# Performance work log

Hardware: AMD Instinct MI355X
Metric: run time of the kernel (lower is better)

## Reference

```python
import jax, jax.numpy as jnp
import numpy as np

B, S, H = 16, 2048, 768
HH = H // 2
C = 64          # num_concepts
L = 4           # num_labels
MIN_SPAN, MAX_SPAN = 3, 20
LEN_BONUS = 0.01
LN_EPS = 1e-5


def _ln(x, g, b):
    m = jnp.mean(x, axis=-1, keepdims=True)
    v = jnp.mean((x - m) ** 2, axis=-1, keepdims=True)
    return (x - m) * jax.lax.rsqrt(v + LN_EPS) * g + b


def _span_mask(scores, valid_len):
    """Vectorized replacement of the per-batch Python span-search loop.
    Replicates torch semantics: iterate span_len (small first), strict '>' update,
    torch.max returns first argmax -> equals argmax over flattened [K,S] array
    with span_len-major ordering."""
    b, s = scores.shape
    cum0 = jnp.concatenate([jnp.zeros((b, 1), scores.dtype),
                            jnp.cumsum(scores, axis=1)], axis=1)          # [B,S+1]
    Ls = jnp.arange(MIN_SPAN, MAX_SPAN + 1)                               # [K]
    starts = jnp.arange(s)                                                # [S]
    ends = starts[None, :] + Ls[:, None]                                  # [K,S]
    ends_c = jnp.minimum(ends, s)
    span_sum = cum0[:, ends_c] - cum0[:, starts][:, None, :]              # [B,K,S]
    avg = span_sum / Ls[None, :, None].astype(scores.dtype) \
        + LEN_BONUS * Ls[None, :, None].astype(scores.dtype) / MAX_SPAN
    valid = ends[None, :, :] <= valid_len[:, None, None]                  # start+len<=valid_len
    avg = jnp.where(valid, avg, -1e30)
    flat_idx = jnp.argmax(avg.reshape(b, -1), axis=1)                     # [B]
    l_idx, start = flat_idx // s, flat_idx % s
    length = Ls[l_idx]
    pos = jnp.arange(s)[None, :]
    span_m = (pos >= start[:, None]) & (pos < (start + length)[:, None])
    short_m = pos < valid_len[:, None]                                    # valid_len<=min_span case
    mask = jnp.where((valid_len <= MIN_SPAN)[:, None], short_m, span_m)
    return jax.lax.stop_gradient(mask.astype(scores.dtype))


def setup_inputs() -> dict:
    key = jax.random.key(0)
    ks = jax.random.split(key, 16)
    std = 0.02
    inp = {
        'inputs_embeds': jax.random.normal(ks[0], (B, S, H), jnp.float32),
        'attention_mask': jnp.ones((B, S), jnp.int32),
        # rationale extractor
        'Wq': jax.random.normal(ks[1], (H, HH), jnp.float32) * std,
        'bq': jnp.zeros((HH,), jnp.float32),
        'Wk': jax.random.normal(ks[2], (H, HH), jnp.float32) * std,
        'bk': jnp.zeros((HH,), jnp.float32),
        'W1': jax.random.normal(ks[3], (H, HH), jnp.float32) * std,
        'b1': jnp.zeros((HH,), jnp.float32),
        'g1': jnp.ones((HH,), jnp.float32),
        'be1': jnp.zeros((HH,), jnp.float32),
        'W2': jax.random.normal(ks[4], (HH, 1), jnp.float32) * 0.01,
        'b2': jnp.zeros((1,), jnp.float32),
        # concept mapper
        'Wc1': jax.random.normal(ks[5], (H, HH), jnp.float32) * std,
        'bc1': jnp.zeros((HH,), jnp.float32),
        'g2': jnp.ones((HH,), jnp.float32),
        'be2': jnp.zeros((HH,), jnp.float32),
        'Wc2': jax.random.normal(ks[6], (HH, C), jnp.float32) * std,
        'bc2': jnp.zeros((C,), jnp.float32),
        'Mint': jnp.zeros((C, C), jnp.float32),  # concept_interactions init zeros
        # classifier (skip connection -> C + H inputs)
        'Wcls': jax.random.normal(ks[7], (C + H, L), jnp.float32) * std,
        'bcls': jnp.zeros((L,), jnp.float32),
    }
    return inp


def reference(inputs_embeds, attention_mask, Wq, bq, Wk, bk, W1, b1, g1, be1, W2, b2,
              Wc1, bc1, g2, be2, Wc2, bc2, Mint, Wcls, bcls):
    x = inputs_embeds                                  # [B,S,H]
    am = attention_mask.astype(bool)                   # [B,S]
    cls_emb = x[:, 0]                                  # [B,H]

    # token scores via self-attention (eval mode: dropout = identity)
    q = x @ Wq + bq                                    # [B,S,HH]
    k = x @ Wk + bk
    attn = jnp.einsum('bsd,btd->bst', q, k) / jnp.sqrt(jnp.float32(HH))
    attn = jnp.where(am[:, None, :], attn, -10000.0)
    p = jax.nn.softmax(attn, axis=-1)
    ctx = jnp.einsum('bst,bth->bsh', p, x)             # [B,S,H]
    h = jax.nn.relu(_ln(ctx @ W1 + b1, g1, be1))
    token_scores = (h @ W2 + b2)[..., 0]               # [B,S]
    token_scores = jnp.where(am, token_scores, -10000.0)

    # span selection + masked mean pooling
    valid_len = jnp.sum(attention_mask.astype(jnp.int32), axis=1)
    rmask = _span_mask(token_scores, valid_len)        # [B,S]
    attended = x * rmask[..., None]
    pooled = jnp.sum(attended, axis=1) / (jnp.sum(rmask, axis=1, keepdims=True) + 1e-6)

    # concept mapper with interactions
    cs = jax.nn.relu(_ln(pooled @ Wc1 + bc1, g2, be2)) @ Wc2 + bc2   # [B,C]
    sym = jax.nn.sigmoid((Mint + Mint.T) / 2)
    cs = cs + cs @ sym
    cprobs = jax.nn.sigmoid(cs)

    logits = jnp.concatenate([cprobs, cls_emb], axis=1) @ Wcls + bcls  # [B,L]
    return logits
```

## Files before the change

kernel.cpp:

```cpp
#include <hip/hip_runtime.h>
#include <hip/hip_bf16.h>

#define Bn  16
#define Sn  2048
#define Hn  768
#define HHn 384

typedef unsigned short ushortT;
typedef unsigned int u32;
typedef __attribute__((ext_vector_type(8))) short short8;
typedef __attribute__((ext_vector_type(4))) short short4v;
typedef __attribute__((ext_vector_type(4))) float f32x4;

static constexpr float SCALE = 0.051031036307982884f;
static constexpr float EPS_PATCH = 0.025f;

static __device__ __forceinline__ float bf2f(ushortT u) {
    return __uint_as_float(((unsigned int)u) << 16);
}
static __device__ __forceinline__ ushortT f2bf(float f) {
    __hip_bfloat16 h = __float2bfloat16(f);
    return *reinterpret_cast<ushortT*>(&h);
}

static __device__ __forceinline__ void gld16(const void* g, void* l) {
    __builtin_amdgcn_global_load_lds(
        (const __attribute__((address_space(1))) u32*)g,
        (__attribute__((address_space(3))) u32*)l, 16, 0, 0);
}
static __device__ __forceinline__ void stage24k(const ushortT* g, unsigned char* l, int tid) {
    const int wid = tid >> 6, lane = tid & 63;
    const unsigned char* gp = (const unsigned char*)g;
#pragma unroll
    for (int i = 0; i < 6; ++i) {
        int blk = i * 4 + wid;
        gld16(gp + blk * 1024 + lane * 16, l + blk * 1024);
    }
}

__global__ __launch_bounds__(256) void convert_x(
    const float* __restrict__ X, ushortT* __restrict__ Xhi, ushortT* __restrict__ Xlo)
{
    size_t i = ((size_t)blockIdx.x * 256 + threadIdx.x) * 4;
    float4 v = *reinterpret_cast<const float4*>(&X[i]);
    short4v h, l;
    float vv[4] = {v.x, v.y, v.z, v.w};
#pragma unroll
    for (int j = 0; j < 4; ++j) {
        ushortT hb = f2bf(vv[j]);
        h[j] = (short)hb;
        l[j] = (short)f2bf(vv[j] - bf2f(hb));
    }
    *reinterpret_cast<short4v*>(&Xhi[i]) = h;
    *reinterpret_cast<short4v*>(&Xlo[i]) = l;
}

__global__ __launch_bounds__(256) void convert_w(
    const float* __restrict__ Wq, const float* __restrict__ Wk, const float* __restrict__ W1,
    ushortT* __restrict__ Wth, ushortT* __restrict__ Wtl)
{
    int t = blockIdx.x * 256 + threadIdx.x;
    int w = t / 36864;
    int r = t % 36864;
    int kg = r / 384;
    int n  = r % 384;
    const float* W = (w == 0) ? Wq : (w == 1) ? Wk : W1;
    short8 h, l;
#pragma unroll
    for (int j = 0; j < 8; ++j) {
        float v = W[(size_t)(kg * 8 + j) * HHn + n];
        ushortT hb = f2bf(v);
        h[j] = (short)hb;
        l[j] = (short)f2bf(v - bf2f(hb));
    }
    size_t off = (size_t)w * 294912 + (size_t)n * 768 + kg * 8;
    *reinterpret_cast<short8*>(&Wth[off]) = h;
    *reinterpret_cast<short8*>(&Wtl[off]) = l;
}

__global__ __launch_bounds__(256, 3) void proj_mfma(
    const ushortT* __restrict__ Xhi, const ushortT* __restrict__ Xlo,
    const ushortT* __restrict__ Wth, const ushortT* __restrict__ Wtl,
    const float* __restrict__ bq, const float* __restrict__ bk, const float* __restrict__ b1,
    ushortT* __restrict__ Qhi, ushortT* __restrict__ Khi, ushortT* __restrict__ Klo,
    ushortT* __restrict__ Uhi, ushortT* __restrict__ Ulo)
{
    __shared__ __align__(16) unsigned char smem[34816];

    const int wsel = blockIdx.z;
    const bool full = (wsel != 0);
    const float* bias = (wsel == 0) ? bq : (wsel == 1) ? bk : b1;
    const ushortT* Wh = Wth + (size_t)wsel * 294912;
    const ushortT* Wl = Wtl + (size_t)wsel * 294912;
    const int m0 = blockIdx.x * 128;
    const int n0 = blockIdx.y * 128;

    const int tid = threadIdx.x, wid = tid >> 6, lane = tid & 63;
    const int quad = lane >> 4, l15 = lane & 15;
    const int mw = (wid >> 1) * 64, nw = (wid & 1) * 64;
    const int r4 = lane >> 2, s2 = lane & 3;
    const int fs = (l15 >> 1) & 3;

    f32x4 acc[4][4];
#pragma unroll
    for (int mt = 0; mt < 4; ++mt)
#pragma unroll
        for (int nt = 0; nt < 4; ++nt) acc[mt][nt] = (f32x4){0.f, 0.f, 0.f, 0.f};

    for (int ks = 0; ks < 24; ++ks) {
        const int k0 = ks * 32;
        __syncthreads();
        {
            const int rb = wid * 32;
#pragma unroll
            for (int h = 0; h < 2; ++h) {
                int row = rb + h * 16 + r4;
                int sw = (row >> 1) & 3;
                size_t gsegA = (size_t)(m0 + row) * 768 + k0 + ((s2 ^ sw) << 3);
                size_t gsegB = (size_t)(n0 + row) * 768 + k0 + ((s2 ^ sw) << 3);
                gld16(&Xhi[gsegA], smem + (rb + h * 16) * 64);
                gld16(&Wh[gsegB],  smem + 16384 + (rb + h * 16) * 64);
                if (full) {
                    gld16(&Xlo[gsegA], smem + 8192  + (rb + h * 16) * 64);
                    gld16(&Wl[gsegB],  smem + 24576 + (rb + h * 16) * 64);
                }
            }
        }
        __syncthreads();

        short8 ah[4], bh[4], al[4], bl[4];
#pragma unroll
        for (int t = 0; t < 4; ++t) {
            int aaddr = (mw + t * 16 + l15) * 64 + ((quad ^ fs) << 4);
            int baddr = (nw + t * 16 + l15) * 64 + ((quad ^ fs) << 4);
            ah[t] = *reinterpret_cast<const short8*>(smem + aaddr);
            bh[t] = *reinterpret_cast<const short8*>(smem + 16384 + baddr);
            if (full) {
                al[t] = *reinterpret_cast<const short8*>(smem + 8192  + aaddr);
                bl[t] = *reinterpret_cast<const short8*>(smem + 24576 + baddr);
            }
        }
#pragma unroll
        for (int mt = 0; mt < 4; ++mt)
#pragma unroll
            for (int nt = 0; nt < 4; ++nt) {
                acc[mt][nt] = __builtin_amdgcn_mfma_f32_16x16x32_bf16(ah[mt], bh[nt], acc[mt][nt], 0, 0, 0);
                if (full) {
                    acc[mt][nt] = __builtin_amdgcn_mfma_f32_16x16x32_bf16(ah[mt], bl[nt], acc[mt][nt], 0, 0, 0);
                    acc[mt][nt] = __builtin_amdgcn_mfma_f32_16x16x32_bf16(al[mt], bh[nt], acc[mt][nt], 0, 0, 0);
                }
            }
    }
    __syncthreads();

    float bv[4];
#pragma unroll
    for (int nt = 0; nt < 4; ++nt) bv[nt] = bias[n0 + nw + nt * 16 + l15];

    if (wsel == 0) {
#pragma unroll
        for (int mt = 0; mt < 4; ++mt)
#pragma unroll
            for (int nt = 0; nt < 4; ++nt)
#pragma unroll
                for (int rg = 0; rg < 4; ++rg) {
                    float v = acc[mt][nt][rg] + bv[nt];
                    *reinterpret_cast<ushortT*>(smem + (mw + mt * 16 + quad * 4 + rg) * 272
                                                     + (nw + nt * 16 + l15) * 2) = f2bf(v);
                }
        __syncthreads();
#pragma unroll
        for (int i = 0; i < 8; ++i) {
            int idx = i * 256 + tid, ml = idx >> 4, cl = idx & 15;
            *reinterpret_cast<uint4*>(&Qhi[(size_t)(m0 + ml) * HHn + n0 + cl * 8]) =
                *reinterpret_cast<const uint4*>(smem + ml * 272 + cl * 16);
        }
    } else if (wsel == 1) {
#pragma unroll
        for (int pass = 0; pass < 2; ++pass) {
            if (pass) __syncthreads();
#pragma unroll
            for (int mt = 0; mt < 4; ++mt)
#pragma unroll
                for (int nt = 0; nt < 4; ++nt)
#pragma unroll
                    for (int rg = 0; rg < 4; ++rg) {
                        float v = acc[mt][nt][rg] + bv[nt];
                        ushortT hb = f2bf(v);
                        ushortT outw = pass ? f2bf(v - bf2f(hb)) : hb;
                        *reinterpret_cast<ushortT*>(smem + (mw + mt * 16 + quad * 4 + rg) * 272
                                                         + (nw + nt * 16 + l15) * 2) = outw;
                    }
            __syncthreads();
            ushortT* dst = pass ? Klo : Khi;
#pragma unroll
            for (int i = 0; i < 8; ++i) {
                int idx = i * 256 + tid, ml = idx >> 4, cl = idx & 15;
                int m = m0 + ml, bb2 = m >> 11, kg = m & 2047, kt = kg >> 6, key = kg & 63;
                int sc_ = ((n0 >> 3) + cl) ^ (key & 7);
                size_t off = ((size_t)(bb2 * 32 + kt) * 64 + key) * 384 + sc_ * 8;
                *reinterpret_cast<uint4*>(&dst[off]) =
                    *reinterpret_cast<const uint4*>(smem + ml * 272 + cl * 16);
            }
        }
    } else {
#pragma unroll
        for (int pass = 0; pass < 2; ++pass) {
            if (pass) __syncthreads();
#pragma unroll
            for (int mt = 0; mt < 4; ++mt)
#pragma unroll
                for (int nt = 0; nt < 4; ++nt) {
                    short4v pk;
#pragma unroll
                    for (int rg = 0; rg < 4; ++rg) {
                        float v = acc[mt][nt][rg] + bv[nt];
                        ushortT hb = f2bf(v);
                        pk[rg] = (short)(pass ? f2bf(v - bf2f(hb)) : hb);
                    }
                    *reinterpret_cast<short4v*>(smem + (nw + nt * 16 + l15) * 272
                                                     + (mw + mt * 16 + quad * 4) * 2) = pk;
                }
            __syncthreads();
            ushortT* dst = pass ? Ulo : Uhi;
#pragma unroll
            for (int i = 0; i < 8; ++i) {
                int idx = i * 256 + tid, dl = idx >> 4, ms = idx & 15;
                int dim = n0 + dl;
                int m = m0 + ms * 8, bb2 = m >> 11, tib = m & 2047;
                int kc = tib >> 5, k8 = (tib >> 3) & 3;
                int sk = k8 ^ (dim & 3);
                size_t off = ((size_t)(bb2 * 64 + kc) * 384 + dim) * 32 + sk * 8;
                *reinterpret_cast<uint4*>(&dst[off]) =
                    *reinterpret_cast<const uint4*>(smem + dl * 272 + ms * 16);
            }
        }
    }
}

__global__ __launch_bounds__(256) void proj_gemm(
    const float* __restrict__ X,
    const float* __restrict__ Wq, const float* __restrict__ bq,
    const float* __restrict__ Wk, const float* __restrict__ bk,
    const float* __restrict__ W1, const float* __restrict__ b1,
    ushortT* __restrict__ Qhi, ushortT* __restrict__ Khi, ushortT* __restrict__ Klo,
    ushortT* __restrict__ Uhi, ushortT* __restrict__ Ulo)
{
    const float* W; const float* bias;
    const int wsel = blockIdx.z;
    if (wsel == 0)      { W = Wq; bias = bq; }
    else if (wsel == 1) { W = Wk; bias = bk; }
    else                { W = W1; bias = b1; }

    const int m0  = blockIdx.x * 128;
    const int n0  = blockIdx.y * 128;
    const int tid = threadIdx.x;
    const int im  = tid >> 4;
    const int jn  = tid & 15;

    __shared__ __align__(16) float sA[16][132];
    __shared__ __align__(16) float sB[16][132];

    float acc[8][8];
#pragma unroll
    for (int i = 0; i < 8; ++i)
#pragma unroll
        for (int j = 0; j < 8; ++j) acc[i][j] = 0.f;

    for (int k0 = 0; k0 < Hn; k0 += 16) {
        __syncthreads();
#pragma unroll
        for (int it = 0; it < 2; ++it) {
            int f = tid + 256 * it;
            int row = f >> 2, k4 = (f & 3) * 4;
            float4 v = *reinterpret_cast<const float4*>(
                &X[(size_t)(m0 + row) * Hn + k0 + k4]);
            sA[k4 + 0][row] = v.x; sA[k4 + 1][row] = v.y;
            sA[k4 + 2][row] = v.z; sA[k4 + 3][row] = v.w;
        }
#pragma unroll
        for (int it = 0; it < 2; ++it) {
            int f = tid + 256 * it;
            int kk = f >> 5, n4 = (f & 31) * 4;
            *reinterpret_cast<float4*>(&sB[kk][n4]) =
                *reinterpret_cast<const float4*>(&W[(size_t)(k0 + kk) * HHn + n0 + n4]);
        }
        __syncthreads();
#pragma unroll
        for (int kk = 0; kk < 16; ++kk) {
            float a[8], bb[8];
            *reinterpret_cast<float4*>(&a[0])  = *reinterpret_cast<const float4*>(&sA[kk][im * 8]);
            *reinterpret_cast<float4*>(&a[4])  = *reinterpret_cast<const float4*>(&sA[kk][im * 8 + 4]);
            *reinterpret_cast<float4*>(&bb[0]) = *reinterpret_cast<const float4*>(&sB[kk][jn * 8]);
            *reinterpret_cast<float4*>(&bb[4]) = *reinterpret_cast<const float4*>(&sB[kk][jn * 8 + 4]);
#pragma unroll
            for (int i = 0; i < 8; ++i)
#pragma unroll
                for (int j = 0; j < 8; ++j) acc[i][j] += a[i] * bb[j];
        }
    }

    if (wsel == 0) {
#pragma unroll
        for (int i = 0; i < 8; ++i) {
            size_t m = (size_t)m0 + im * 8 + i;
            int nb = n0 + jn * 8;
            short8 hv;
#pragma unroll
            for (int j = 0; j < 8; ++j) hv[j] = (short)f2bf(acc[i][j] + bias[nb + j]);
            *reinterpret_cast<short8*>(&Qhi[m * HHn + nb]) = hv;
        }
    } else if (wsel == 1) {
        const int bb = m0 >> 11;
        const int bibase = m0 & 2047;
#pragma unroll
        for (int i = 0; i < 8; ++i) {
            int kg = bibase + im * 8 + i;
            int kt = kg >> 6, key = kg & 63;
            size_t rowoff = ((size_t)(bb * 32 + kt) * 64 + key) * 384;
            int sc_ = ((n0 >> 3) + jn) ^ (key & 7);
            short8 hv, lv;
#pragma unroll
            for (int j = 0; j < 8; ++j) {
                float v = acc[i][j] + bias[n0 + jn * 8 + j];
                ushortT hb = f2bf(v);
                hv[j] = (short)hb;
                lv[j] = (short)f2bf(v - bf2f(hb));
            }
            *reinterpret_cast<short8*>(&Khi[rowoff + sc_ * 8]) = hv;
            *reinterpret_cast<short8*>(&Klo[rowoff + sc_ * 8]) = lv;
        }
    } else {
        const int bb = m0 >> 11;
        const int tib = (m0 & 2047) + im * 8;
        const int kc = tib >> 5, k8 = (tib >> 3) & 3;
        const size_t cbase = (size_t)(bb * 64 + kc) * 384;
#pragma unroll
        for (int j = 0; j < 8; ++j) {
            int dim = n0 + jn * 8 + j;
            int sk = k8 ^ (dim & 3);
            float bvv = bias[dim];
            short8 hv, lv;
#pragma unroll
            for (int i = 0; i < 8; ++i) {
                float v = acc[i][j] + bvv;
                ushortT hb = f2bf(v);
                hv[i] = (short)hb;
                lv[i] = (short)f2bf(v - bf2f(hb));
            }
            size_t off = (cbase + dim) * 32 + sk * 8;
            *reinterpret_cast<short8*>(&Uhi[off]) = hv;
            *reinterpret_cast<short8*>(&Ulo[off]) = lv;
        }
    }
}

__global__ __launch_bounds__(256, 2) void attn_mfma(
    const ushortT* Qg, const ushortT* __restrict__ Kp, const ushortT* __restrict__ Up,
    const int* __restrict__ am, ushortT* Hp)
{
    __shared__ __align__(16) unsigned char smem[81920];
    ushortT* sP = (ushortT*)(smem + 73728);

    const int tid  = threadIdx.x;
    const int wid  = tid >> 6;
    const int lane = tid & 63;
    const int quad = lane >> 4;
    const int l15  = lane & 15;
    const int b    = blockIdx.y;
    const int q0   = blockIdx.x * 64;
    const size_t rowbase = (size_t)b * Sn + q0;
    const int* amb = am + b * Sn;

    const ushortT* Kbase = Kp + (size_t)b * 32 * 64 * 384;
    const ushortT* Ubase = Up + (size_t)b * 64 * 12288;

    const int r0 = wid * 16;
    short8 qf[12];
#pragma unroll
    for (int ks = 0; ks < 12; ++ks)
        qf[ks] = *reinterpret_cast<const short8*>(
            &Qg[(rowbase + r0 + l15) * HHn + ks * 32 + quad * 8]);

    f32x4 o[4][6];
#pragma unroll
    for (int rt = 0; rt < 4; ++rt)
#pragma unroll
        for (int dt = 0; dt < 6; ++dt) o[rt][dt] = (f32x4){0.f, 0.f, 0.f, 0.f};
    float denacc[4] = {0.f, 0.f, 0.f, 0.f};

    int ia = 0, ibx = 24576, ic = 49152;
    stage24k(Kbase, smem + ia, tid);
    stage24k(Kbase + 12288, smem + ibx, tid);
    __syncthreads();

    const int d0 = wid * 96;

    for (int kt = 0; kt < 32; ++kt) {
        stage24k(Ubase + (size_t)(kt * 2) * 12288, smem + ic, tid);

        f32x4 sc[4];
#pragma unroll
        for (int ct = 0; ct < 4; ++ct) sc[ct] = (f32x4){0.f, 0.f, 0.f, 0.f};
#pragma unroll
        for (int ks = 0; ks < 12; ++ks) {
#pragma unroll
            for (int ct = 0; ct < 4; ++ct) {
                int kl = (ct & 1) * 16 + l15;
                const unsigned char* Bk = smem + ((ct < 2) ? ia : ibx);
                short8 bf = *reinterpret_cast<const short8*>(
                    Bk + kl * 768 + ((((ks << 2) + quad) ^ (kl & 7)) << 4));
                sc[ct] = __builtin_amdgcn_mfma_f32_16x16x32_bf16(qf[ks], bf, sc[ct], 0, 0, 0);
            }
        }

        float dp[4] = {0.f, 0.f, 0.f, 0.f};
#pragma unroll
        for (int ct = 0; ct < 4; ++ct) {
            int col = ct * 16 + l15;
            float mval = (amb[kt * 64 + col] != 0) ? 1.f : 0.f;
#pragma unroll
            for (int rg = 0; rg < 4; ++rg) {
                int row = r0 + quad * 4 + rg;
                float p = __expf(sc[ct][rg] * SCALE) * mval;
                sP[row * 64 + (((col >> 3) ^ (row & 7)) << 3) + (col & 7)] = f2bf(p);
                dp[rg] += p;
            }
        }
#pragma unroll
        for (int off = 1; off < 16; off <<= 1)
#pragma unroll
            for (int rg = 0; rg < 4; ++rg) dp[rg] += __shfl_xor(dp[rg], off, 16);
#pragma unroll
        for (int rg = 0; rg < 4; ++rg) denacc[rg] += dp[rg];

        __syncthreads();

        stage24k(Ubase + (size_t)(kt * 2 + 1) * 12288, smem + ia, tid);
        if (kt < 31) stage24k(Kbase + (size_t)(kt + 1) * 24576, smem + ibx, tid);

        {
            const unsigned char* Bu = smem + ic;
            short8 pa[4];
#pragma unroll
            for (int rt = 0; rt < 4; ++rt)
                pa[rt] = *reinterpret_cast<const short8*>(
                    &sP[(16 * rt + l15) * 64 + ((quad ^ (l15 & 7)) << 3)]);
#pragma unroll
            for (int dt = 0; dt < 6; ++dt) {
                short8 u = *reinterpret_cast<const short8*>(
                    Bu + (d0 + 16 * dt + l15) * 64 + ((quad ^ (l15 & 3)) << 4));
#pragma unroll
                for (int rt = 0; rt < 4; ++rt)
                    o[rt][dt] = __builtin_amdgcn_mfma_f32_16x16x32_bf16(pa[rt], u, o[rt][dt], 0, 0, 0);
            }
        }
        __syncthreads();

        if (kt < 31) stage24k(Kbase + (size_t)(kt + 1) * 24576 + 12288, smem + ic, tid);

        {
            const unsigned char* Bu = smem + ia;
            short8 pa[4];
#pragma unroll
            for (int rt = 0; rt < 4; ++rt)
                pa[rt] = *reinterpret_cast<const short8*>(
                    &sP[(16 * rt + l15) * 64 + (((4 + quad) ^ (l15 & 7)) << 3)]);
#pragma unroll
            for (int dt = 0; dt < 6; ++dt) {
                short8 u = *reinterpret_cast<const short8*>(
                    Bu + (d0 + 16 * dt + l15) * 64 + ((quad ^ (l15 & 3)) << 4));
#pragma unroll
                for (int rt = 0; rt < 4; ++rt)
                    o[rt][dt] = __builtin_amdgcn_mfma_f32_16x16x32_bf16(pa[rt], u, o[rt][dt], 0, 0, 0);
            }
        }
        __syncthreads();

        int t = ia; ia = ibx; ibx = ic; ic = t;
    }

    float* sDenF = (float*)smem;
    if (l15 == 0) {
#pragma unroll
        for (int rg = 0; rg < 4; ++rg) sDenF[r0 + quad * 4 + rg] = denacc[rg];
    }
    __syncthreads();
    ushortT* sHp = (ushortT*)(smem + 512);
#pragma unroll
    for (int rt = 0; rt < 4; ++rt)
#pragma unroll
        for (int rg = 0; rg < 4; ++rg) {
            int row = rt * 16 + quad * 4 + rg;
            float inv = 1.f / sDenF[row];
#pragma unroll
            for (int dt = 0; dt < 6; ++dt)
                sHp[row * 384 + d0 + dt * 16 + l15] = f2bf(o[rt][dt][rg] * inv);
        }
    __syncthreads();
#pragma unroll
    for (int i = 0; i < 12; ++i) {
        int idx = i * 256 + tid;
        *reinterpret_cast<uint4*>(&Hp[rowbase * HHn + idx * 8]) =
            *reinterpret_cast<const uint4*>(&sHp[idx * 8]);
    }
}

__global__ __launch_bounds__(256) void ln_score_kernel(
    const ushortT* __restrict__ Hp, const float* __restrict__ g1, const float* __restrict__ be1,
    const float* __restrict__ W2, const float* __restrict__ b2,
    const int* __restrict__ am, float* __restrict__ scores, int* __restrict__ count)
{
    if (blockIdx.x == 0 && threadIdx.x == 0) *count = 0;
    const int row  = blockIdx.x * 4 + (threadIdx.x >> 6);
    const int lane = threadIdx.x & 63;
    const ushortT* x = Hp + (size_t)row * HHn;
    float v[6];
#pragma unroll
    for (int j = 0; j < 6; ++j) v[j] = bf2f(x[lane + 64 * j]);
    float s = 0.f;
#pragma unroll
    for (int j = 0; j < 6; ++j) s += v[j];
#pragma unroll
    for (int off = 32; off > 0; off >>= 1) s += __shfl_xor(s, off, 64);
    const float mean = s * (1.0f / 384.0f);
    float q = 0.f;
#pragma unroll
    for (int j = 0; j < 6; ++j) { float d = v[j] - mean; q += d * d; }
#pragma unroll
    for (int off = 32; off > 0; off >>= 1) q += __shfl_xor(q, off, 64);
    const float rstd = rsqrtf(q * (1.0f / 384.0f) + 1e-5f);
    float part = 0.f;
#pragma unroll
    for (int j = 0; j < 6; ++j) {
        int d = lane + 64 * j;
        float h = (v[j] - mean) * rstd * g1[d] + be1[d];
        h = fmaxf(h, 0.f);
        part += h * W2[d];
    }
#pragma unroll
    for (int off = 32; off > 0; off >>= 1) part += __shfl_xor(part, off, 64);
    if (lane == 0) {
        float scv = part + b2[0];
        if (am[row] == 0) scv = -10000.0f;
        scores[row] = scv;
    }
}

__global__ __launch_bounds__(256) void span_flag_kernel(
    const float* __restrict__ scores, const int* __restrict__ am,
    int* __restrict__ list, int* __restrict__ count)
{
    __shared__ float cum[Sn + 1];
    __shared__ float psum[257];
    __shared__ float bval[256];
    __shared__ int   sred[256];
    __shared__ int   sInfo[1];
    __shared__ float sBest;
    __shared__ unsigned char sflag[Sn];

    const int b = blockIdx.x, tid = threadIdx.x;
    for (int i = tid; i < Sn; i += 256) sflag[i] = 0;

    int vl = 0;
    for (int i = tid; i < Sn; i += 256) vl += am[b * Sn + i];
    sred[tid] = vl;
    __syncthreads();
    if (tid == 0) { int t = 0; for (int i = 0; i < 256; ++i) t += sred[i]; sInfo[0] = t; }
    __syncthreads();
    const int valid_len = sInfo[0];

    float loc[8]; float tot = 0.f;
#pragma unroll
    for (int k2 = 0; k2 < 8; ++k2) { loc[k2] = scores[b * Sn + tid * 8 + k2]; tot += loc[k2]; }
    psum[tid + 1] = tot;
    __syncthreads();
    if (tid == 0) {
        psum[0] = 0.f;
        float r = 0.f;
        for (int i = 1; i <= 256; ++i) { float t = psum[i]; psum[i] = r + t; r += t; }
    }
    __syncthreads();
    {
        float r = (tid == 0) ? 0.f : psum[tid];
        if (tid == 0) cum[0] = 0.f;
#pragma unroll
        for (int k2 = 0; k2 < 8; ++k2) { r += loc[k2]; cum[tid * 8 + k2 + 1] = r; }
    }
    __syncthreads();

    float bv = -3.0e30f;
    for (int flat = tid; flat < 18 * Sn; flat += 256) {
        int l = flat >> 11, st = flat & (Sn - 1), L = 3 + l, end = st + L;
        float val;
        if (end <= valid_len) {
            int ec = end < Sn ? end : Sn;
            val = (cum[ec] - cum[st]) / (float)L + (0.01f * (float)L) / 20.0f;
        } else val = -1.0e30f;
        if (val > bv) bv = val;
    }
    bval[tid] = bv;
    __syncthreads();
    if (tid == 0) {
        float best = bval[0];
        for (int i = 1; i < 256; ++i) if (bval[i] > best) best = bval[i];
        sBest = best;
    }
    __syncthreads();

    if (valid_len > 3) {
        const float thr = sBest - EPS_PATCH;
        for (int flat = tid; flat < 18 * Sn; flat += 256) {
            int l = flat >> 11, st = flat & (Sn - 1), L = 3 + l, end = st + L;
            if (end <= valid_len) {
                int ec = end < Sn ? end : Sn;
                float val = (cum[ec] - cum[st]) / (float)L + (0.01f * (float)L) / 20.0f;
                if (val >= thr)
                    for (int t = st; t < end; ++t) sflag[t] = 1;
            }
        }
        __syncthreads();
        for (int t = tid; t < Sn; t += 256)
            if (sflag[t]) { int idx = atomicAdd(count, 1); list[idx] = (b << 16) | t; }
    }
}

static __device__ __forceinline__ float block_sum256(float v, float* sws, int tid)
{
#pragma unroll
    for (int off = 32; off > 0; off >>= 1) v += __shfl_xor(v, off, 64);
    __syncthreads();
    if ((tid & 63) == 0) sws[tid >> 6] = v;
    __syncthreads();
    return sws[0] + sws[1] + sws[2] + sws[3];
}

__global__ __launch_bounds__(256) void patch_kernel(
    const int* __restrict__ list, const int* __restrict__ count,
    const float* __restrict__ X, const float* __restrict__ Wq, const float* __restrict__ bq,
    const ushortT* __restrict__ Khi, const ushortT* __restrict__ Klo,
    const ushortT* __restrict__ Uhi, const ushortT* __restrict__ Ulo,
    const float* __restrict__ g1, const float* __restrict__ be1,
    const float* __restrict__ W2, const float* __restrict__ b2,
    const int* __restrict__ am, float* __restrict__ scores)
{
    __shared__ float sx[Hn];
    __shared__ float sq[HHn];
    __shared__ float sp[Sn];
    __shared__ float sws[4];
    const int tid = threadIdx.x;
    const int n = *count;

    for (int li = blockIdx.x; li < n; li += gridDim.x) {
        int e = list[li];
        int b = e >> 16, t = e & 0xffff;
        __syncthreads();
        for (int d = tid; d < Hn; d += 256) sx[d] = X[((size_t)b * Sn + t) * Hn + d];
        __syncthreads();
        for (int d = tid; d < HHn; d += 256) {
            float a = bq[d];
            for (int k = 0; k < Hn; ++k) a += sx[k] * Wq[(size_t)k * HHn + d];
            sq[d] = a;
        }
        __syncthreads();
        float dpart = 0.f;
        for (int j = tid; j < Sn; j += 256) {
            float p = 0.f;
            if (am[b * Sn + j] != 0) {
                int kt = j >> 6, key = j & 63, kk7 = key & 7;
                size_t ro = ((size_t)(b * 32 + kt) * 64 + key) * 384;
                const ushortT* kh = &Khi[ro];
                const ushortT* kl = &Klo[ro];
                float s = 0.f;
                for (int c = 0; c < 48; ++c) {
                    int dbase = (c ^ kk7) << 3;
                    for (int ee = 0; ee < 8; ++ee)
                        s += sq[dbase + ee] * (bf2f(kh[c * 8 + ee]) + bf2f(kl[c * 8 + ee]));
                }
                p = expf(s * SCALE);
            }
            sp[j] = p; dpart += p;
        }
        const float den = block_sum256(dpart, sws, tid);

        float cown[2] = {0.f, 0.f};
        {
            int ii = 0;
            for (int d = tid; d < HHn; d += 256, ++ii) {
                int d3 = d & 3;
                float c = 0.f;
                for (int kc = 0; kc < 64; ++kc) {
                    size_t ub = ((size_t)(b * 64 + kc) * 384 + d) * 32;
                    const ushortT* uh = &Uhi[ub];
                    const ushortT* ul = &Ulo[ub];
                    for (int k8 = 0; k8 < 4; ++k8) {
                        int sk = k8 ^ d3;
                        int j0 = kc * 32 + k8 * 8;
                        for (int ee = 0; ee < 8; ++ee)
                            c += sp[j0 + ee] * (bf2f(uh[sk * 8 + ee]) + bf2f(ul[sk * 8 + ee]));
                    }
                }
                cown[ii] = c / den;
            }
        }
        float ssum = cown[0] + cown[1];
        const float mean = block_sum256(ssum, sws, tid) * (1.0f / 384.0f);
        float vsum = 0.f;
        {
            int ii = 0;
            for (int d = tid; d < HHn; d += 256, ++ii) {
                float dv = cown[ii] - mean; vsum += dv * dv;
            }
        }
        const float var = block_sum256(vsum, sws, tid) * (1.0f / 384.0f);
        const float rstd = rsqrtf(var + 1e-5f);
        float spart = 0.f;
        {
            int ii = 0;
            for (int d = tid; d < HHn; d += 256, ++ii) {
                float h = (cown[ii] - mean) * rstd * g1[d] + be1[d];
                h = fmaxf(h, 0.f);
                spart += h * W2[d];
            }
        }
        const float sc = block_sum256(spart, sws, tid) + b2[0];
        if (tid == 0)
            scores[b * Sn + t] = (am[b * Sn + t] != 0) ? sc : -10000.0f;
        __syncthreads();
    }
}

__global__ __launch_bounds__(256) void span_pool_kernel(
    const float* __restrict__ scores, const int* __restrict__ am,
    const float* __restrict__ X, float* __restrict__ pooled)
{
    __shared__ float cum[Sn + 1];
    __shared__ float psum[257];
    __shared__ float bval[256];
    __shared__ int   bidx[256];
    __shared__ int   sred[256];
    __shared__ int   sInfo[2];

    const int b = blockIdx.x, tid = threadIdx.x;

    int vl = 0;
    for (int i = tid; i < Sn; i += 256) vl += am[b * Sn + i];
    sred[tid] = vl;
    __syncthreads();
    if (tid == 0) { int t = 0; for (int i = 0; i < 256; ++i) t += sred[i]; sInfo[0] = t; }
    __syncthreads();
    const int valid_len = sInfo[0];

    float loc[8]; float tot = 0.f;
#pragma unroll
    for (int k2 = 0; k2 < 8; ++k2) { loc[k2] = scores[b * Sn + tid * 8 + k2]; tot += loc[k2]; }
    psum[tid + 1] = tot;
    __syncthreads();
    if (tid == 0) {
        psum[0] = 0.f;
        float r = 0.f;
        for (int i = 1; i <= 256; ++i) { float t = psum[i]; psum[i] = r + t; r += t; }
    }
    __syncthreads();
    {
        float r = (tid == 0) ? 0.f : psum[tid];
        if (tid == 0) cum[0] = 0.f;
#pragma unroll
        for (int k2 = 0; k2 < 8; ++k2) { r += loc[k2]; cum[tid * 8 + k2 + 1] = r; }
    }
    __syncthreads();

    float bv = -3.0e30f; int bi = 0x7fffffff;
    for (int flat = tid; flat < 18 * Sn; flat += 256) {
        int l  = flat >> 11;
        int st = flat & (Sn - 1);
        int L  = 3 + l;
        int end = st + L;
        float val;
        if (end <= valid_len) {
            int ec = end < Sn ? end : Sn;
            val = (cum[ec] - cum[st]) / (float)L + (0.01f * (float)L) / 20.0f;
        } else val = -1.0e30f;
        if (val > bv) { bv = val; bi = flat; }
    }
    bval[tid] = bv; bidx[tid] = bi;
    __syncthreads();
    if (tid == 0) {
        float best = bval[0]; int besti = bidx[0];
        for (int i = 1; i < 256; ++i) {
            if (bval[i] > best || (bval[i] == best && bidx[i] < besti)) {
                best = bval[i]; besti = bidx[i];
            }
        }
        int st, len;
        if (valid_len <= 3) { st = 0; len = valid_len; }
        else { int l = besti >> 11; st = besti & (Sn - 1); len = 3 + l; }
        sInfo[0] = st; sInfo[1] = len;
    }
    __syncthreads();
    const int st = sInfo[0], len = sInfo[1];
    for (int d = tid; d < Hn; d += 256) {
        float s2 = 0.f;
        for (int i = 0; i < len; ++i) s2 += X[((size_t)b * Sn + st + i) * Hn + d];
        pooled[b * Hn + d] = s2 / ((float)len + 1e-6f);
    }
}

__global__ __launch_bounds__(384) void head_kernel(
    const float* __restrict__ pooled,
    const float* __restrict__ Wc1, const float* __restrict__ bc1,
    const float* __restrict__ g2, const float* __restrict__ be2,
    const float* __restrict__ Wc2, const float* __restrict__ bc2,
    const float* __restrict__ Mint,
    const float* __restrict__ Wcls, const float* __restrict__ bcls,
    const float* __restrict__ X, float* __restrict__ out)
{
    __shared__ float sp[768];
    __shared__ float sh[384];
    __shared__ float scs[64];
    __shared__ float scp[64];
    __shared__ float red[6];
    __shared__ float stat;

    const int b = blockIdx.x, tid = threadIdx.x;
    sp[tid]       = pooled[b * Hn + tid];
    sp[tid + 384] = pooled[b * Hn + 384 + tid];
    __syncthreads();

    float z = bc1[tid];
    for (int k2 = 0; k2 < Hn; ++k2) z += sp[k2] * Wc1[(size_t)k2 * HHn + tid];

    float s = z;
#pragma unroll
    for (int off = 32; off > 0; off >>= 1) s += __shfl_xor(s, off, 64);
    if ((tid & 63) == 0) red[tid >> 6] = s;
    __syncthreads();
    if (tid == 0) stat = (red[0] + red[1] + red[2] + red[3] + red[4] + red[5]) * (1.0f / 384.0f);
    __syncthreads();
    const float mean = stat;
    float dv = z - mean;
    float qq = dv * dv;
#pragma unroll
    for (int off = 32; off > 0; off >>= 1) qq += __shfl_xor(qq, off, 64);
    if ((tid & 63) == 0) red[tid >> 6] = qq;
    __syncthreads();
    if (tid == 0) stat = (red[0] + red[1] + red[2] + red[3] + red[4] + red[5]) * (1.0f / 384.0f);
    __syncthreads();
    const float rstd = rsqrtf(stat + 1e-5f);
    float h = fmaxf(dv * rstd * g2[tid] + be2[tid], 0.f);
    sh[tid] = h;
    __syncthreads();
    if (tid < 64) {
        float c = bc2[tid];
        for (int k2 = 0; k2 < HHn; ++k2) c += sh[k2] * Wc2[k2 * 64 + tid];
        scs[tid] = c;
    }
    __syncthreads();
    if (tid < 64) {
        float a2 = scs[tid];
        for (int c2 = 0; c2 < 64; ++c2) {
            float m   = 0.5f * (Mint[c2 * 64 + tid] + Mint[tid * 64 + c2]);
            float sym = 1.0f / (1.0f + expf(-m));
            a2 += scs[c2] * sym;
        }
        scp[tid] = 1.0f / (1.0f + expf(-a2));
    }
    __syncthreads();
    if (tid < 4) {
        float lg = bcls[tid];
        for (int c2 = 0; c2 < 64; ++c2) lg += scp[c2] * Wcls[c2 * 4 + tid];
        const float* cls = X + (size_t)b * Sn * Hn;
        for (int d2 = 0; d2 < Hn; ++d2) lg += cls[d2] * Wcls[(64 + d2) * 4 + tid];
        out[b * 4 + tid] = lg;
    }
}

extern "C" void kernel_launch(void* const* d_in, const int* in_sizes, int n_in,
                              void* d_out, int out_size, void* d_ws, size_t ws_size,
                              hipStream_t stream)
{
    const float* X    = (const float*)d_in[0];
    const int*   am   = (const int*)  d_in[1];
    const float* Wq   = (const float*)d_in[2];
    const float* bq   = (const float*)d_in[3];
    const float* Wk   = (const float*)d_in[4];
    const float* bk   = (const float*)d_in[5];
    const float* W1   = (const float*)d_in[6];
    const float* b1   = (const float*)d_in[7];
    const float* g1   = (const float*)d_in[8];
    const float* be1  = (const float*)d_in[9];
    const float* W2   = (const float*)d_in[10];
    const float* b2   = (const float*)d_in[11];
    const float* Wc1  = (const float*)d_in[12];
    const float* bc1  = (const float*)d_in[13];
    const float* g2   = (const float*)d_in[14];
    const float* be2  = (const float*)d_in[15];
    const float* Wc2  = (const float*)d_in[16];
    const float* bc2  = (const float*)d_in[17];
    const float* Mint = (const float*)d_in[18];
    const float* Wcls = (const float*)d_in[19];
    const float* bcls = (const float*)d_in[20];

    const size_t NTb = (size_t)Bn * Sn * HHn;
    ushortT* Qhi  = (ushortT*)d_ws;
    ushortT* Kp   = Qhi + NTb;
    ushortT* Kplo = Kp  + NTb;
    ushortT* Upp  = Kplo + NTb;
    ushortT* Uplo = Upp + NTb;
    float* scores = (float*)(Uplo + NTb);
    float* pooled = scores + (size_t)Bn * Sn;
    int* list     = (int*)(pooled + (size_t)Bn * Hn);
    int* count    = list + Bn * Sn;
    ushortT* Xhi  = (ushortT*)(count + 4);
    const size_t NX = (size_t)Bn * Sn * Hn;
    ushortT* Xlo  = Xhi + NX;
    ushortT* Wth  = Xlo + NX;
    ushortT* Wtl  = Wth + 3 * 294912;
    const size_t NEED = (size_t)((unsigned char*)(Wtl + 3 * 294912) - (unsigned char*)d_ws);

    ushortT* Hp   = Qhi;

    if (ws_size >= NEED) {
        convert_x<<<24576, 256, 0, stream>>>(X, Xhi, Xlo);
        convert_w<<<432, 256, 0, stream>>>(Wq, Wk, W1, Wth, Wtl);
        proj_mfma<<<dim3(256, 3, 3), 256, 0, stream>>>(Xhi, Xlo, Wth, Wtl, bq, bk, b1,
                                                       Qhi, Kp, Kplo, Upp, Uplo);
    } else {
        proj_gemm<<<dim3(256, 3, 3), 256, 0, stream>>>(X, Wq, bq, Wk, bk, W1, b1,
                                                       Qhi, Kp, Kplo, Upp, Uplo);
    }
    attn_mfma<<<dim3(Sn / 64, Bn), 256, 0, stream>>>(Qhi, Kp, Upp, am, Hp);
    ln_score_kernel<<<(Bn * Sn) / 4, 256, 0, stream>>>(Hp, g1, be1, W2, b2, am, scores, count);
    span_flag_kernel<<<Bn, 256, 0, stream>>>(scores, am, list, count);
    patch_kernel<<<1024, 256, 0, stream>>>(list, count, X, Wq, bq, Kp, Kplo, Upp, Uplo,
                                           g1, be1, W2, b2, am, scores);
    span_pool_kernel<<<Bn, 256, 0, stream>>>(scores, am, X, pooled);
    head_kernel<<<Bn, 384, 0, stream>>>(pooled, Wc1, bc1, g2, be2, Wc2, bc2,
                                        Mint, Wcls, bcls, X, (float*)d_out);
}
```

Measured before the change: 1.240 ms.

## Widen patch kernel to 512 threads with vectorized loads, tighten patch threshold

The patch kernel recomputes exact fp32 token scores for near-best span candidates. It now uses 512 threads per block, loads K and U rows as 16-byte short8 vectors, and reads the query and probabilities as float4 from shared memory. The QK loop is restructured so each thread accumulates four keys across the 48 chunks. The patch threshold also drops from 0.025 to 0.02, so fewer tokens get recomputed, which narrows the margin for correcting bf16-split scoring errors near the argmax.

```diff
diff --git a/kernel.cpp b/kernel.cpp
--- a/kernel.cpp
+++ b/kernel.cpp
@@ -13,7 +13,7 @@
 typedef __attribute__((ext_vector_type(4))) float f32x4;
 
 static constexpr float SCALE = 0.051031036307982884f;
-static constexpr float EPS_PATCH = 0.025f;
+static constexpr float EPS_PATCH = 0.02f;
 
 static __device__ __forceinline__ float bf2f(ushortT u) {
     return __uint_as_float(((unsigned int)u) << 16);
@@ -625,17 +625,20 @@
     }
 }
 
-static __device__ __forceinline__ float block_sum256(float v, float* sws, int tid)
+static __device__ __forceinline__ float block_sum512(float v, float* sws, int tid)
 {
 #pragma unroll
     for (int off = 32; off > 0; off >>= 1) v += __shfl_xor(v, off, 64);
     __syncthreads();
     if ((tid & 63) == 0) sws[tid >> 6] = v;
     __syncthreads();
-    return sws[0] + sws[1] + sws[2] + sws[3];
-}
-
-__global__ __launch_bounds__(256) void patch_kernel(
+    float r = 0.f;
+#pragma unroll
+    for (int i = 0; i < 8; ++i) r += sws[i];
+    return r;
+}
+
+__global__ __launch_bounds__(512) void patch_kernel(
     const int* __restrict__ list, const int* __restrict__ count,
     const float* __restrict__ X, const float* __restrict__ Wq, const float* __restrict__ bq,
     const ushortT* __restrict__ Khi, const ushortT* __restrict__ Klo,
@@ -644,10 +647,10 @@
     const float* __restrict__ W2, const float* __restrict__ b2,
     const int* __restrict__ am, float* __restrict__ scores)
 {
-    __shared__ float sx[Hn];
-    __shared__ float sq[HHn];
-    __shared__ float sp[Sn];
-    __shared__ float sws[4];
+    __shared__ __align__(16) float sx[Hn];
+    __shared__ __align__(16) float sq[HHn];
+    __shared__ __align__(16) float sp[Sn];
+    __shared__ float sws[8];
     const int tid = threadIdx.x;
     const int n = *count;
 
@@ -655,75 +658,96 @@
         int e = list[li];
         int b = e >> 16, t = e & 0xffff;
         __syncthreads();
-        for (int d = tid; d < Hn; d += 256) sx[d] = X[((size_t)b * Sn + t) * Hn + d];
-        __syncthreads();
-        for (int d = tid; d < HHn; d += 256) {
-            float a = bq[d];
-            for (int k = 0; k < Hn; ++k) a += sx[k] * Wq[(size_t)k * HHn + d];
-            sq[d] = a;
+        for (int d = tid; d < Hn; d += 512) sx[d] = X[((size_t)b * Sn + t) * Hn + d];
+        __syncthreads();
+        if (tid < HHn) {
+            float a = bq[tid];
+            for (int k4 = 0; k4 < 192; ++k4) {
+                float4 xv = *reinterpret_cast<const float4*>(&sx[k4 * 4]);
+                a += xv.x * Wq[(size_t)(k4 * 4 + 0) * HHn + tid]
+                   + xv.y * Wq[(size_t)(k4 * 4 + 1) * HHn + tid]
+                   + xv.z * Wq[(size_t)(k4 * 4 + 2) * HHn + tid]
+                   + xv.w * Wq[(size_t)(k4 * 4 + 3) * HHn + tid];
+            }
+            sq[tid] = a;
         }
         __syncthreads();
         float dpart = 0.f;
-        for (int j = tid; j < Sn; j += 256) {
-            float p = 0.f;
-            if (am[b * Sn + j] != 0) {
-                int kt = j >> 6, key = j & 63, kk7 = key & 7;
-                size_t ro = ((size_t)(b * 32 + kt) * 64 + key) * 384;
-                const ushortT* kh = &Khi[ro];
-                const ushortT* kl = &Klo[ro];
-                float s = 0.f;
-                for (int c = 0; c < 48; ++c) {
-                    int dbase = (c ^ kk7) << 3;
-                    for (int ee = 0; ee < 8; ++ee)
-                        s += sq[dbase + ee] * (bf2f(kh[c * 8 + ee]) + bf2f(kl[c * 8 + ee]));
+        {
+            float acc[4] = {0.f, 0.f, 0.f, 0.f};
+            size_t ro[4]; int kk7[4];
+#pragma unroll
+            for (int i = 0; i < 4; ++i) {
+                int j = tid + i * 512;
+                int kt = j >> 6, key = j & 63;
+                ro[i] = ((size_t)(b * 32 + kt) * 64 + key) * 384;
+                kk7[i] = key & 7;
+            }
+            for (int g = 0; g < 48; ++g) {
+                float4 qa = *reinterpret_cast<const float4*>(&sq[g * 8]);
+                float4 qb = *reinterpret_cast<const float4*>(&sq[g * 8 + 4]);
+#pragma unroll
+                for (int i = 0; i < 4; ++i) {
+                    int c = g ^ kk7[i];
+                    short8 kh = *reinterpret_cast<const short8*>(&Khi[ro[i] + c * 8]);
+                    short8 kl = *reinterpret_cast<const short8*>(&Klo[ro[i] + c * 8]);
+                    acc[i] += qa.x * (bf2f((ushortT)kh[0]) + bf2f((ushortT)kl[0]))
+                            + qa.y * (bf2f((ushortT)kh[1]) + bf2f((ushortT)kl[1]))
+                            + qa.z * (bf2f((ushortT)kh[2]) + bf2f((ushortT)kl[2]))
+                            + qa.w * (bf2f((ushortT)kh[3]) + bf2f((ushortT)kl[3]))
+                            + qb.x * (bf2f((ushortT)kh[4]) + bf2f((ushortT)kl[4]))
+                            + qb.y * (bf2f((ushortT)kh[5]) + bf2f((ushortT)kl[5]))
+                            + qb.z * (bf2f((ushortT)kh[6]) + bf2f((ushortT)kl[6]))
+                            + qb.w * (bf2f((ushortT)kh[7]) + bf2f((ushortT)kl[7]));
                 }
-                p = expf(s * SCALE);
-            }
-            sp[j] = p; dpart += p;
-        }
-        const float den = block_sum256(dpart, sws, tid);
-
-        float cown[2] = {0.f, 0.f};
-        {
-            int ii = 0;
-            for (int d = tid; d < HHn; d += 256, ++ii) {
-                int d3 = d & 3;
-                float c = 0.f;
-                for (int kc = 0; kc < 64; ++kc) {
-                    size_t ub = ((size_t)(b * 64 + kc) * 384 + d) * 32;
-                    const ushortT* uh = &Uhi[ub];
-                    const ushortT* ul = &Ulo[ub];
-                    for (int k8 = 0; k8 < 4; ++k8) {
-                        int sk = k8 ^ d3;
-                        int j0 = kc * 32 + k8 * 8;
-                        for (int ee = 0; ee < 8; ++ee)
-                            c += sp[j0 + ee] * (bf2f(uh[sk * 8 + ee]) + bf2f(ul[sk * 8 + ee]));
-                    }
+            }
+#pragma unroll
+            for (int i = 0; i < 4; ++i) {
+                int j = tid + i * 512;
+                float p = (am[b * Sn + j] != 0) ? expf(acc[i] * SCALE) : 0.f;
+                sp[j] = p; dpart += p;
+            }
+        }
+        const float den = block_sum512(dpart, sws, tid);
+
+        float cown = 0.f;
+        if (tid < HHn) {
+            const int d = tid, d3 = d & 3;
+            float c = 0.f;
+            for (int kc = 0; kc < 64; ++kc) {
+                size_t ub = ((size_t)(b * 64 + kc) * 384 + d) * 32;
+#pragma unroll
+                for (int sk = 0; sk < 4; ++sk) {
+                    int k8 = sk ^ d3;
+                    int j0 = kc * 32 + k8 * 8;
+                    short8 uh = *reinterpret_cast<const short8*>(&Uhi[ub + sk * 8]);
+                    short8 ul = *reinterpret_cast<const short8*>(&Ulo[ub + sk * 8]);
+                    float4 pa = *reinterpret_cast<const float4*>(&sp[j0]);
+                    float4 pb = *reinterpret_cast<const float4*>(&sp[j0 + 4]);
+                    c += pa.x * (bf2f((ushortT)uh[0]) + bf2f((ushortT)ul[0]))
+                       + pa.y * (bf2f((ushortT)uh[1]) + bf2f((ushortT)ul[1]))
+                       + pa.z * (bf2f((ushortT)uh[2]) + bf2f((ushortT)ul[2]))
+                       + pa.w * (bf2f((ushortT)uh[3]) + bf2f((ushortT)ul[3]))
+                       + pb.x * (bf2f((ushortT)uh[4]) + bf2f((ushortT)ul[4]))
+                       + pb.y * (bf2f((ushortT)uh[5]) + bf2f((ushortT)ul[5]))
+                       + pb.z * (bf2f((ushortT)uh[6]) + bf2f((ushortT)ul[6]))
+                       + pb.w * (bf2f((ushortT)uh[7]) + bf2f((ushortT)ul[7]));
                 }
-                cown[ii] = c / den;
-            }
-        }
-        float ssum = cown[0] + cown[1];
-        const float mean = block_sum256(ssum, sws, tid) * (1.0f / 384.0f);
+            }
+            cown = c / den;
+        }
+        const float mean = block_sum512(cown, sws, tid) * (1.0f / 384.0f);
         float vsum = 0.f;
-        {
-            int ii = 0;
-            for (int d = tid; d < HHn; d += 256, ++ii) {
-                float dv = cown[ii] - mean; vsum += dv * dv;
-            }
-        }
-        const float var = block_sum256(vsum, sws, tid) * (1.0f / 384.0f);
+        if (tid < HHn) { float dv = cown - mean; vsum = dv * dv; }
+        const float var = block_sum512(vsum, sws, tid) * (1.0f / 384.0f);
         const float rstd = rsqrtf(var + 1e-5f);
         float spart = 0.f;
-        {
-            int ii = 0;
-            for (int d = tid; d < HHn; d += 256, ++ii) {
-                float h = (cown[ii] - mean) * rstd * g1[d] + be1[d];
-                h = fmaxf(h, 0.f);
-                spart += h * W2[d];
-            }
-        }
-        const float sc = block_sum256(spart, sws, tid) + b2[0];
+        if (tid < HHn) {
+            float h = (cown - mean) * rstd * g1[tid] + be1[tid];
+            h = fmaxf(h, 0.f);
+            spart = h * W2[tid];
+        }
+        const float sc = block_sum512(spart, sws, tid) + b2[0];
         if (tid == 0)
             scores[b * Sn + t] = (am[b * Sn + t] != 0) ? sc : -10000.0f;
         __syncthreads();
@@ -932,7 +956,7 @@
     attn_mfma<<<dim3(Sn / 64, Bn), 256, 0, stream>>>(Qhi, Kp, Upp, am, Hp);
     ln_score_kernel<<<(Bn * Sn) / 4, 256, 0, stream>>>(Hp, g1, be1, W2, b2, am, scores, count);
     span_flag_kernel<<<Bn, 256, 0, stream>>>(scores, am, list, count);
-    patch_kernel<<<1024, 256, 0, stream>>>(list, count, X, Wq, bq, Kp, Kplo, Upp, Uplo,
+    patch_kernel<<<1024, 512, 0, stream>>>(list, count, X, Wq, bq, Kp, Kplo, Upp, Uplo,
                                            g1, be1, W2, b2, am, scores);
     span_pool_kernel<<<Bn, 256, 0, stream>>>(scores, am, X, pooled);
     head_kernel<<<Bn, 384, 0, stream>>>(pooled, Wc1, bc1, g2, be2, Wc2, bc2,
```

Result: no change. 1.264 ms (+1.9%).
